# Kernel optimization log

Measured on AMD Instinct MI355X. Metric: run time of the kernel, lower is better.

## Reference

```python
import jax, jax.numpy as jnp
import numpy as np

ORDER = 25
L = ORDER + 1
K = 64
B = 262144
N_ITER = 8
WEIGHT_FLOOR = 1e-05
VAR_FLOOR = 1e-06
LOG_PI = L * float(np.log(2.0 * np.pi))  # (order+1)*log(2*pi)


def setup_inputs() -> dict:
    key = jax.random.key(0)
    k1, k2 = jax.random.split(key)
    x = jax.random.normal(k1, (B, L), dtype=jnp.float32)
    mu0 = jax.random.normal(k2, (K, L), dtype=jnp.float32)      # torch.randn(K, L)
    w0 = jnp.ones((K,), dtype=jnp.float32)                      # normalized to 1/K in reference
    sigma0 = jnp.ones((K, L), dtype=jnp.float32)                # diagonal of eye(L)
    return {"x": x, "w0": w0, "mu0": mu0, "sigma0": sigma0}


def _em_step(x, w, mu, sig):
    # ---- E-step (diag covariance path of the torch module) ----
    log_det = jnp.sum(jnp.log(sig), axis=-1)                    # [K]
    prec = 1.0 / sig                                            # [K,L]
    # mahala[b,k] = sum_l (x[b,l]-mu[k,l])^2 * prec[k,l]
    # expanded quadratic form to avoid materializing [B,K,L]
    mahala = ((x * x) @ prec.T
              - 2.0 * (x @ (mu * prec).T)
              + jnp.sum(mu * mu * prec, axis=-1))               # [B,K]
    numer = jnp.log(w) - 0.5 * (LOG_PI + log_det + mahala)      # [B,K]
    denom = jax.scipy.special.logsumexp(numer, axis=-1, keepdims=True)
    posterior = jnp.exp(numer - denom)                          # [B,K]
    ll = jnp.sum(denom)
    # ---- M-step (alpha == 0) ----
    z = jnp.sum(posterior, axis=0)                              # [K]
    w_new = z / B
    zinv = 1.0 / z
    # weight flooring + renormalization
    w_new = jnp.maximum(w_new, WEIGHT_FLOOR)
    sum_floor = WEIGHT_FLOOR * K
    a = (1.0 - sum_floor) / (jnp.sum(w_new) - sum_floor)
    b = WEIGHT_FLOOR * (1.0 - a)
    w_new = a * w_new + b
    px = posterior.T @ x                                        # [K,L]
    mu_new = px * zinv[:, None]
    pxx = posterior.T @ (x * x)                                 # [K,L]
    sig_new = pxx * zinv[:, None] - mu_new * mu_new
    sig_new = jnp.maximum(sig_new, VAR_FLOOR)                   # variance flooring
    return w_new, mu_new, sig_new, ll


def reference(x, w0, mu0, sigma0):
    w = w0 / jnp.sum(w0)                                        # == 1/K for ones init

    def body(carry, _):
        w, mu, sig, _ = carry
        w, mu, sig, ll = _em_step(x, w, mu, sig)
        return (w, mu, sig, ll), None

    init = (w, mu0, sigma0, jnp.zeros((), dtype=jnp.float32))
    (w, mu, sig, ll), _ = jax.lax.scan(body, init, None, length=N_ITER)
    sigma = jax.vmap(jnp.diag)(sig)                             # [K,L,L] diagonal covariances
    return w, mu, sigma, ll
```

## Files before the change

### kernel.cpp

```cpp
#include <hip/hip_runtime.h>
#include <math.h>

typedef _Float16 f16x2 __attribute__((ext_vector_type(2)));
typedef _Float16 f16x8 __attribute__((ext_vector_type(8)));
typedef float f32x16 __attribute__((ext_vector_type(16)));
typedef unsigned int uint4v __attribute__((ext_vector_type(4)));

namespace {
constexpr int LDIM = 26;
constexpr int KDIM = 64;
constexpr int NSAMP = 262144;
constexpr int NITER = 8;
constexpr float WFLOOR = 1e-5f;
constexpr float VFLOOR = 1e-6f;
constexpr float LOG2PI_TERM = 47.784803726642976f;
constexpr float L2E = 1.44269504088896340736f;
constexpr float LN2 = 0.69314718055994530942f;

constexpr int ACC_STRIDE = 53;
constexpr int ACC_N = KDIM * ACC_STRIDE + 1;
constexpr int NCOPIES = 8;
constexpr int WROW = 36;
constexpr int NBLK = 1024;
constexpr int PART_STRIDE = 3408;
constexpr int XROW = 20;
}

__device__ float g_partial[NBLK * PART_STRIDE];
__device__ float g_accum[NCOPIES * ACC_N];
__device__ float g_w[KDIM];
__device__ float g_mu[KDIM * LDIM];
__device__ float g_sig[KDIM * LDIM];
__device__ float g_ll[1];
__device__ __align__(16) unsigned g_coef[KDIM * WROW];
__device__ __align__(16) unsigned g_x16[NSAMP * XROW];

__device__ __forceinline__ unsigned pkrtz(float a, float b) {
  return __builtin_bit_cast(unsigned, __builtin_amdgcn_cvt_pkrtz(a, b));
}
__device__ __forceinline__ unsigned sqr16(unsigned u) {
  f16x2 a = __builtin_bit_cast(f16x2, u);
  a = a * a;
  return __builtin_bit_cast(unsigned, a);
}
__device__ __forceinline__ f16x8 ld8h(const unsigned* p) {
  uint4v v = *(const uint4v*)p;
  return __builtin_bit_cast(f16x8, v);
}
__device__ __forceinline__ f32x16 mfma16(f16x8 a, f16x8 b, f32x16 c) {
  return __builtin_amdgcn_mfma_f32_32x32x16_f16(a, b, c, 0, 0, 0);
}
__device__ __forceinline__ void gload16(const void* g, void* l) {
  __builtin_amdgcn_global_load_lds(
      (const __attribute__((address_space(1))) unsigned*)g,
      (__attribute__((address_space(3))) unsigned*)l, 16, 0, 0);
}

__device__ void pack_row(int k, float w, const float* mu, const float* sg, unsigned* wp) {
  float A[LDIM], Bv[LDIM];
  float logdet = 0.f, q = 0.f;
#pragma unroll
  for (int l = 0; l < LDIM; ++l) {
    float pr = 1.0f / sg[l];
    logdet += __logf(sg[l]);
    A[l] = -0.5f * pr;
    Bv[l] = mu[l] * pr;
    q = __builtin_fmaf(mu[l] * mu[l], pr, q);
  }
  float C = __logf(w) - 0.5f * (LOG2PI_TERM + logdet + q);
  float Chi = (float)__builtin_amdgcn_cvt_pkrtz(C, 0.0f)[0];
  float Clo = C - Chi;
  unsigned* row = wp + k * WROW;
#define CF(f) ((f) < 26 ? A[(f)] : (f) < 52 ? Bv[(f) - 26] : (f) == 52 ? C : (f) == 53 ? Clo : 0.0f)
#pragma unroll
  for (int D = 0; D < 32; ++D) row[D] = pkrtz(CF(2 * D), CF(2 * D + 1));
#undef CF
#pragma unroll
  for (int D = 32; D < 36; ++D) row[D] = 0u;
}

__global__ void prep_coef(const float* __restrict__ w0, const float* __restrict__ mu0,
                          const float* __restrict__ sig0) {
  const int k = threadIdx.x;
  float wv = w0[k];
  float s = wv;
#pragma unroll
  for (int d = 1; d < 64; d <<= 1) s += __shfl_xor(s, d, 64);
  float w = wv / s;
  float mu[LDIM], sg[LDIM];
#pragma unroll
  for (int l = 0; l < LDIM; ++l) {
    mu[l] = mu0[k * LDIM + l];
    sg[l] = sig0[k * LDIM + l];
  }
  pack_row(k, w, mu, sg, g_coef);
}

__global__ void pack16(const float* __restrict__ x) {
  const int total = NSAMP * XROW;
  for (int idx = blockIdx.x * 256 + threadIdx.x; idx < total; idx += gridDim.x * 256) {
    const int s = idx / XROW, j = idx % XROW;
    unsigned v = 0u;
    if (j < 13) {
      float2 p = *(const float2*)(x + (size_t)s * LDIM + 2 * j);
      v = pkrtz(p.x, p.y);
    }
    g_x16[idx] = v;
  }
}

__global__ __launch_bounds__(128, 2) void em_mfma() {
  __shared__ __align__(16) unsigned char pool[16384];
  __shared__ __align__(16) unsigned stage[2][2][32 * XROW];

  const int tid = threadIdx.x;
  const int lane = tid & 63;
  const int warp = tid >> 6;
  const int sl = lane & 31;
  const int h = lane >> 5;

  unsigned short* XTs = (unsigned short*)&pool[warp * 4096];
  unsigned short* SQs = (unsigned short*)&pool[warp * 4096 + 2048];
  unsigned short* PT0s = (unsigned short*)&pool[8192 + warp * 4096];
  unsigned short* PT1s = (unsigned short*)&pool[8192 + warp * 4096 + 2048];
  const unsigned* XTd = (const unsigned*)XTs;
  const unsigned* SQd = (const unsigned*)SQs;
  const unsigned* PT0d = (const unsigned*)PT0s;
  const unsigned* PT1d = (const unsigned*)PT1s;

  f32x16 aX0 = {0,0,0,0,0,0,0,0,0,0,0,0,0,0,0,0};
  f32x16 aX1 = {0,0,0,0,0,0,0,0,0,0,0,0,0,0,0,0};
  f32x16 aQ0 = {0,0,0,0,0,0,0,0,0,0,0,0,0,0,0,0};
  f32x16 aQ1 = {0,0,0,0,0,0,0,0,0,0,0,0,0,0,0,0};
  float llacc = 0.f;

  const int sbase = blockIdx.x * 256 + warp * 128;
  const int rowbase0 = sl * WROW;
  const int rowbase1 = (32 + sl) * WROW;

  f16x8 ca00 = ld8h(g_coef + rowbase0 + 0 + 4 * h);
  f16x8 ca01 = ld8h(g_coef + rowbase0 + 8 + 4 * h);
  f16x8 ca02 = ld8h(g_coef + rowbase0 + 16 + 4 * h);
  f16x8 ca03 = ld8h(g_coef + rowbase0 + 24 + 4 * h);
  f16x8 ca10 = ld8h(g_coef + rowbase1 + 0 + 4 * h);
  f16x8 ca11 = ld8h(g_coef + rowbase1 + 8 + 4 * h);
  f16x8 ca12 = ld8h(g_coef + rowbase1 + 16 + 4 * h);
  f16x8 ca13 = ld8h(g_coef + rowbase1 + 24 + 4 * h);

  auto stage_tile = [&](int tt) {
    const uint4v* tb = (const uint4v*)(g_x16 + (size_t)(sbase + 32 * tt) * XROW);
    char* db = (char*)&stage[warp][tt & 1][0];
    gload16(tb + lane, db + (size_t)lane * 16);
    gload16(tb + 64 + lane, db + 1024 + (size_t)lane * 16);
    if (lane < 32) gload16(tb + 128 + lane, db + 2048 + (size_t)lane * 16);
  };

  stage_tile(0);

#pragma unroll
  for (int t = 0; t < 4; ++t) {
    asm volatile("s_waitcnt vmcnt(0)" ::: "memory");

    if (t < 3) stage_tile(t + 1);

    unsigned xhu[13], squ[13];
    {
      const unsigned* srow = &stage[warp][t & 1][sl * XROW];
      uint4v r0 = *(const uint4v*)(srow);
      uint4v r1 = *(const uint4v*)(srow + 4);
      uint4v r2 = *(const uint4v*)(srow + 8);
      unsigned r12 = srow[12];
      xhu[0] = r0[0]; xhu[1] = r0[1]; xhu[2] = r0[2]; xhu[3] = r0[3];
      xhu[4] = r1[0]; xhu[5] = r1[1]; xhu[6] = r1[2]; xhu[7] = r1[3];
      xhu[8] = r2[0]; xhu[9] = r2[1]; xhu[10] = r2[2]; xhu[11] = r2[3];
      xhu[12] = r12;
#pragma unroll
      for (int j = 0; j < 13; ++j) squ[j] = sqr16(xhu[j]);
    }

    {
      unsigned short* Ts = h ? SQs : XTs;
#pragma unroll
      for (int c = 0; c < LDIM; ++c) {
        unsigned src = h ? squ[c >> 1] : xhu[c >> 1];
        unsigned v = (c & 1) ? (src >> 16) : (src & 0xffffu);
        Ts[(c * 32 + sl) ^ ((c & 7) << 3)] = (unsigned short)v;
      }
      Ts[(26 * 32 + sl) ^ ((26 & 7) << 3)] = h ? (unsigned short)0 : (unsigned short)0x3C00;
    }

    f32x16 e0 = {0,0,0,0,0,0,0,0,0,0,0,0,0,0,0,0};
    f32x16 e1 = {0,0,0,0,0,0,0,0,0,0,0,0,0,0,0,0};
    {
      uint4v b0 = {h ? squ[4] : squ[0], h ? squ[5] : squ[1],
                   h ? squ[6] : squ[2], h ? squ[7] : squ[3]};
      uint4v b1 = {h ? squ[12] : squ[8], h ? xhu[0] : squ[9],
                   h ? xhu[1] : squ[10], h ? xhu[2] : squ[11]};
      uint4v b2 = {h ? xhu[7] : xhu[3], h ? xhu[8] : xhu[4],
                   h ? xhu[9] : xhu[5], h ? xhu[10] : xhu[6]};
      uint4v b3 = {h ? 0u : xhu[11], h ? 0u : xhu[12],
                   h ? 0u : 0x3C003C00u, 0u};
      f16x8 fb0 = __builtin_bit_cast(f16x8, b0);
      f16x8 fb1 = __builtin_bit_cast(f16x8, b1);
      f16x8 fb2 = __builtin_bit_cast(f16x8, b2);
      f16x8 fb3 = __builtin_bit_cast(f16x8, b3);
      e0 = mfma16(ca00, fb0, e0);
      e1 = mfma16(ca10, fb0, e1);
      e0 = mfma16(ca01, fb1, e0);
      e1 = mfma16(ca11, fb1, e1);
      e0 = mfma16(ca02, fb2, e0);
      e1 = mfma16(ca12, fb2, e1);
      e0 = mfma16(ca03, fb3, e0);
      e1 = mfma16(ca13, fb3, e1);
    }

    float m8[8];
#pragma unroll
    for (int r = 0; r < 8; ++r)
      m8[r] = fmaxf(fmaxf(e0[r], e0[r + 8]), fmaxf(e1[r], e1[r + 8]));
#pragma unroll
    for (int d = 4; d > 0; d >>= 1)
#pragma unroll
      for (int r = 0; r < d; ++r) m8[r] = fmaxf(m8[r], m8[r + d]);
    const float M = fmaxf(m8[0], __shfl_xor(m8[0], 32));
    const float mL = M * L2E;
#pragma unroll
    for (int r = 0; r < 16; ++r) {
      e0[r] = __builtin_amdgcn_exp2f(__builtin_fmaf(e0[r], L2E, -mL));
      e1[r] = __builtin_amdgcn_exp2f(__builtin_fmaf(e1[r], L2E, -mL));
    }
    float s8[8];
#pragma unroll
    for (int r = 0; r < 8; ++r)
      s8[r] = (e0[r] + e0[r + 8]) + (e1[r] + e1[r + 8]);
#pragma unroll
    for (int d = 4; d > 0; d >>= 1)
#pragma unroll
      for (int r = 0; r < d; ++r) s8[r] += s8[r + d];
    const float SS = s8[0] + __shfl_xor(s8[0], 32);
    const float scale = __builtin_amdgcn_rcpf(SS);
    llacc += M + __builtin_amdgcn_logf(SS) * LN2;

#pragma unroll
    for (int r = 0; r < 16; ++r) {
      const int row = (r & 3) + 8 * (r >> 2) + 4 * h;
      const int idx = (row * 32 + sl) ^ ((row & 7) << 3);
      _Float16 p0 = (_Float16)(e0[r] * scale);
      _Float16 p1 = (_Float16)(e1[r] * scale);
      PT0s[idx] = __builtin_bit_cast(unsigned short, p0);
      PT1s[idx] = __builtin_bit_cast(unsigned short, p1);
    }

#pragma unroll
    for (int ks = 0; ks < 2; ++ks) {
      const int off = 8 * ks + 4 * h;
      const int swz = (sl & 7) << 2;
      f16x8 a0 = ld8h(&PT0d[(sl * 16 + off) ^ swz]);
      f16x8 a1 = ld8h(&PT1d[(sl * 16 + off) ^ swz]);
      f16x8 bx = ld8h(&XTd[(sl * 16 + off) ^ swz]);
      f16x8 bq = ld8h(&SQd[(sl * 16 + off) ^ swz]);
      aX0 = mfma16(a0, bx, aX0);
      aQ0 = mfma16(a0, bq, aQ0);
      aX1 = mfma16(a1, bx, aX1);
      aQ1 = mfma16(a1, bq, aQ1);
    }
  }

  __syncthreads();
  float* red = (float*)&pool[0];
  float llw = llacc * 0.5f;
#pragma unroll
  for (int d = 1; d < 64; d <<= 1) llw += __shfl_xor(llw, d, 64);
  if (warp == 0) {
#pragma unroll
    for (int r = 0; r < 16; ++r) {
      const int row = (r & 3) + 8 * (r >> 2) + 4 * h;
      if (sl < 26) {
        red[row * ACC_STRIDE + 1 + sl] = aX0[r];
        red[row * ACC_STRIDE + 27 + sl] = aQ0[r];
        red[(row + 32) * ACC_STRIDE + 1 + sl] = aX1[r];
        red[(row + 32) * ACC_STRIDE + 27 + sl] = aQ1[r];
      } else if (sl == 26) {
        red[row * ACC_STRIDE] = aX0[r];
        red[(row + 32) * ACC_STRIDE] = aX1[r];
      }
    }
    if (lane == 0) red[KDIM * ACC_STRIDE] = llw;
  }
  __syncthreads();
  if (warp == 1) {
    float* pb = g_partial + (size_t)blockIdx.x * PART_STRIDE;
#pragma unroll
    for (int r = 0; r < 16; ++r) {
      const int row = (r & 3) + 8 * (r >> 2) + 4 * h;
      if (sl < 26) {
        pb[row * ACC_STRIDE + 1 + sl] = red[row * ACC_STRIDE + 1 + sl] + aX0[r];
        pb[row * ACC_STRIDE + 27 + sl] = red[row * ACC_STRIDE + 27 + sl] + aQ0[r];
        pb[(row + 32) * ACC_STRIDE + 1 + sl] = red[(row + 32) * ACC_STRIDE + 1 + sl] + aX1[r];
        pb[(row + 32) * ACC_STRIDE + 27 + sl] = red[(row + 32) * ACC_STRIDE + 27 + sl] + aQ1[r];
      } else if (sl == 26) {
        pb[row * ACC_STRIDE] = red[row * ACC_STRIDE] + aX0[r];
        pb[(row + 32) * ACC_STRIDE] = red[(row + 32) * ACC_STRIDE] + aX1[r];
      }
    }
    if (lane == 0) pb[KDIM * ACC_STRIDE] = red[KDIM * ACC_STRIDE] + llw;
  }
}

__global__ void reduce_partials() {
  const int i = blockIdx.x * 256 + threadIdx.x;
  if (i >= ACC_N) return;
  const int cy = blockIdx.y;
  const float* p = g_partial + (size_t)cy * 128 * PART_STRIDE + i;
  float s = 0.f;
#pragma unroll 8
  for (int j = 0; j < 128; ++j) s += p[(size_t)j * PART_STRIDE];
  g_accum[cy * ACC_N + i] = s;
}

__global__ void finalize_k() {
  const int k = threadIdx.x;
  float vals[ACC_STRIDE];
#pragma unroll
  for (int j = 0; j < ACC_STRIDE; ++j) vals[j] = 0.f;
  float llsum = 0.f;
  for (int cp = 0; cp < NCOPIES; ++cp) {
    const float* a = g_accum + cp * ACC_N;
#pragma unroll
    for (int j = 0; j < ACC_STRIDE; ++j) vals[j] += a[k * ACC_STRIDE + j];
    llsum += a[KDIM * ACC_STRIDE];
  }
  float z = vals[0];
  float wn = z * (1.0f / NSAMP);
  float wf = fmaxf(wn, WFLOOR);
  float S = wf;
#pragma unroll
  for (int d = 1; d < 64; d <<= 1) S += __shfl_xor(S, d, 64);
  const float sf = WFLOOR * KDIM;
  float a = (1.0f - sf) / (S - sf);
  float b = WFLOOR * (1.0f - a);
  float w = a * wf + b;
  g_w[k] = w;
  float zinv = 1.0f / z;
  float muk[LDIM], sgk[LDIM];
#pragma unroll
  for (int l = 0; l < LDIM; ++l) {
    float m = vals[1 + l] * zinv;
    float s2 = fmaxf(__builtin_fmaf(-m, m, vals[27 + l] * zinv), VFLOOR);
    muk[l] = m;
    sgk[l] = s2;
    g_mu[k * LDIM + l] = m;
    g_sig[k * LDIM + l] = s2;
  }
  if (k == 0) g_ll[0] = llsum;
  pack_row(k, w, muk, sgk, g_coef);
}

__global__ void writeout(float* __restrict__ out) {
  const int i = blockIdx.x * 256 + threadIdx.x;
  if (i < 64) {
    out[i] = g_w[i];
  } else if (i < 64 + KDIM * LDIM) {
    out[i] = g_mu[i - 64];
  } else if (i < 64 + KDIM * LDIM + KDIM * LDIM * LDIM) {
    int t = i - (64 + KDIM * LDIM);
    int k = t / (LDIM * LDIM);
    int r = t % (LDIM * LDIM);
    int ii = r / LDIM;
    int jj = r % LDIM;
    out[i] = (ii == jj) ? g_sig[k * LDIM + ii] : 0.f;
  } else if (i == 64 + KDIM * LDIM + KDIM * LDIM * LDIM) {
    out[i] = g_ll[0];
  }
}

extern "C" void kernel_launch(void* const* d_in, const int* in_sizes, int n_in,
                              void* d_out, int out_size, void* d_ws, size_t ws_size,
                              hipStream_t stream) {
  (void)in_sizes; (void)n_in; (void)d_ws; (void)ws_size; (void)out_size;
  const float* x   = (const float*)d_in[0];
  const float* w0  = (const float*)d_in[1];
  const float* mu0 = (const float*)d_in[2];
  const float* sg0 = (const float*)d_in[3];
  float* out = (float*)d_out;

  prep_coef<<<1, 64, 0, stream>>>(w0, mu0, sg0);
  pack16<<<2048, 256, 0, stream>>>(x);
  for (int it = 0; it < NITER; ++it) {
    em_mfma<<<NBLK, 128, 0, stream>>>();
    reduce_partials<<<dim3(14, 8), 256, 0, stream>>>();
    finalize_k<<<1, 64, 0, stream>>>();
  }
  const int nout = 64 + KDIM * LDIM + KDIM * LDIM * LDIM + 1;
  writeout<<<(nout + 255) / 256, 256, 0, stream>>>(out);
}
```

Before: 318.9 us.

## Use four waves per block with direct register loads instead of LDS staging

The E/M-step kernel now runs 256 threads per block, with each wave handling 64 samples (two tiles) instead of 128 (four tiles). Samples go straight from global memory into registers, replacing the double-buffered global_load_lds staging. The block reduction becomes two parallel LDS pairwise reductions followed by a cooperative coalesced write of the partials. The aim is more waves in flight to hide latency and a cheaper, coalesced partial write-out, at the cost of more LDS per block and an extra barrier.

```diff
diff --git a/kernel.cpp b/kernel.cpp
--- a/kernel.cpp
+++ b/kernel.cpp
@@ -50,11 +50,6 @@
 __device__ __forceinline__ f32x16 mfma16(f16x8 a, f16x8 b, f32x16 c) {
   return __builtin_amdgcn_mfma_f32_32x32x16_f16(a, b, c, 0, 0, 0);
 }
-__device__ __forceinline__ void gload16(const void* g, void* l) {
-  __builtin_amdgcn_global_load_lds(
-      (const __attribute__((address_space(1))) unsigned*)g,
-      (__attribute__((address_space(3))) unsigned*)l, 16, 0, 0);
-}
 
 __device__ void pack_row(int k, float w, const float* mu, const float* sg, unsigned* wp) {
   float A[LDIM], Bv[LDIM];
@@ -109,9 +104,8 @@
   }
 }
 
-__global__ __launch_bounds__(128, 2) void em_mfma() {
-  __shared__ __align__(16) unsigned char pool[16384];
-  __shared__ __align__(16) unsigned stage[2][2][32 * XROW];
+__global__ __launch_bounds__(256, 3) void em_mfma() {
+  __shared__ __align__(16) unsigned char pool[32768];
 
   const int tid = threadIdx.x;
   const int lane = tid & 63;
@@ -119,10 +113,10 @@
   const int sl = lane & 31;
   const int h = lane >> 5;
 
-  unsigned short* XTs = (unsigned short*)&pool[warp * 4096];
-  unsigned short* SQs = (unsigned short*)&pool[warp * 4096 + 2048];
-  unsigned short* PT0s = (unsigned short*)&pool[8192 + warp * 4096];
-  unsigned short* PT1s = (unsigned short*)&pool[8192 + warp * 4096 + 2048];
+  unsigned short* XTs = (unsigned short*)&pool[warp * 8192];
+  unsigned short* SQs = (unsigned short*)&pool[warp * 8192 + 2048];
+  unsigned short* PT0s = (unsigned short*)&pool[warp * 8192 + 4096];
+  unsigned short* PT1s = (unsigned short*)&pool[warp * 8192 + 6144];
   const unsigned* XTd = (const unsigned*)XTs;
   const unsigned* SQd = (const unsigned*)SQs;
   const unsigned* PT0d = (const unsigned*)PT0s;
@@ -134,7 +128,7 @@
   f32x16 aQ1 = {0,0,0,0,0,0,0,0,0,0,0,0,0,0,0,0};
   float llacc = 0.f;
 
-  const int sbase = blockIdx.x * 256 + warp * 128;
+  const int sbase = blockIdx.x * 256 + warp * 64;
   const int rowbase0 = sl * WROW;
   const int rowbase1 = (32 + sl) * WROW;
 
@@ -147,36 +141,26 @@
   f16x8 ca12 = ld8h(g_coef + rowbase1 + 16 + 4 * h);
   f16x8 ca13 = ld8h(g_coef + rowbase1 + 24 + 4 * h);
 
-  auto stage_tile = [&](int tt) {
-    const uint4v* tb = (const uint4v*)(g_x16 + (size_t)(sbase + 32 * tt) * XROW);
-    char* db = (char*)&stage[warp][tt & 1][0];
-    gload16(tb + lane, db + (size_t)lane * 16);
-    gload16(tb + 64 + lane, db + 1024 + (size_t)lane * 16);
-    if (lane < 32) gload16(tb + 128 + lane, db + 2048 + (size_t)lane * 16);
-  };
-
-  stage_tile(0);
-
-#pragma unroll
-  for (int t = 0; t < 4; ++t) {
-    asm volatile("s_waitcnt vmcnt(0)" ::: "memory");
-
-    if (t < 3) stage_tile(t + 1);
-
+  uint4v ra[2][3];
+  unsigned rb[2];
+#pragma unroll
+  for (int t = 0; t < 2; ++t) {
+    const uint4v* rp = (const uint4v*)(g_x16 + (size_t)(sbase + 32 * t + sl) * XROW);
+    ra[t][0] = rp[0];
+    ra[t][1] = rp[1];
+    ra[t][2] = rp[2];
+    rb[t] = ((const unsigned*)rp)[12];
+  }
+
+#pragma unroll
+  for (int t = 0; t < 2; ++t) {
     unsigned xhu[13], squ[13];
-    {
-      const unsigned* srow = &stage[warp][t & 1][sl * XROW];
-      uint4v r0 = *(const uint4v*)(srow);
-      uint4v r1 = *(const uint4v*)(srow + 4);
-      uint4v r2 = *(const uint4v*)(srow + 8);
-      unsigned r12 = srow[12];
-      xhu[0] = r0[0]; xhu[1] = r0[1]; xhu[2] = r0[2]; xhu[3] = r0[3];
-      xhu[4] = r1[0]; xhu[5] = r1[1]; xhu[6] = r1[2]; xhu[7] = r1[3];
-      xhu[8] = r2[0]; xhu[9] = r2[1]; xhu[10] = r2[2]; xhu[11] = r2[3];
-      xhu[12] = r12;
-#pragma unroll
-      for (int j = 0; j < 13; ++j) squ[j] = sqr16(xhu[j]);
-    }
+    xhu[0] = ra[t][0][0]; xhu[1] = ra[t][0][1]; xhu[2] = ra[t][0][2]; xhu[3] = ra[t][0][3];
+    xhu[4] = ra[t][1][0]; xhu[5] = ra[t][1][1]; xhu[6] = ra[t][1][2]; xhu[7] = ra[t][1][3];
+    xhu[8] = ra[t][2][0]; xhu[9] = ra[t][2][1]; xhu[10] = ra[t][2][2]; xhu[11] = ra[t][2][3];
+    xhu[12] = rb[t];
+#pragma unroll
+    for (int j = 0; j < 13; ++j) squ[j] = sqr16(xhu[j]);
 
     {
       unsigned short* Ts = h ? SQs : XTs;
@@ -266,12 +250,15 @@
     }
   }
 
+  float* redA = (float*)&pool[0];
+  float* redB = (float*)&pool[16384];
+  float llw = llacc * 0.5f;
+#pragma unroll
+  for (int d = 1; d < 64; d <<= 1) llw += __shfl_xor(llw, d, 64);
+
   __syncthreads();
-  float* red = (float*)&pool[0];
-  float llw = llacc * 0.5f;
-#pragma unroll
-  for (int d = 1; d < 64; d <<= 1) llw += __shfl_xor(llw, d, 64);
-  if (warp == 0) {
+  if (warp == 0 || warp == 2) {
+    float* red = (warp == 0) ? redA : redB;
 #pragma unroll
     for (int r = 0; r < 16; ++r) {
       const int row = (r & 3) + 8 * (r >> 2) + 4 * h;
@@ -288,22 +275,27 @@
     if (lane == 0) red[KDIM * ACC_STRIDE] = llw;
   }
   __syncthreads();
-  if (warp == 1) {
-    float* pb = g_partial + (size_t)blockIdx.x * PART_STRIDE;
+  if (warp == 1 || warp == 3) {
+    float* red = (warp == 1) ? redA : redB;
 #pragma unroll
     for (int r = 0; r < 16; ++r) {
       const int row = (r & 3) + 8 * (r >> 2) + 4 * h;
       if (sl < 26) {
-        pb[row * ACC_STRIDE + 1 + sl] = red[row * ACC_STRIDE + 1 + sl] + aX0[r];
-        pb[row * ACC_STRIDE + 27 + sl] = red[row * ACC_STRIDE + 27 + sl] + aQ0[r];
-        pb[(row + 32) * ACC_STRIDE + 1 + sl] = red[(row + 32) * ACC_STRIDE + 1 + sl] + aX1[r];
-        pb[(row + 32) * ACC_STRIDE + 27 + sl] = red[(row + 32) * ACC_STRIDE + 27 + sl] + aQ1[r];
+        red[row * ACC_STRIDE + 1 + sl] += aX0[r];
+        red[row * ACC_STRIDE + 27 + sl] += aQ0[r];
+        red[(row + 32) * ACC_STRIDE + 1 + sl] += aX1[r];
+        red[(row + 32) * ACC_STRIDE + 27 + sl] += aQ1[r];
       } else if (sl == 26) {
-        pb[row * ACC_STRIDE] = red[row * ACC_STRIDE] + aX0[r];
-        pb[(row + 32) * ACC_STRIDE] = red[(row + 32) * ACC_STRIDE] + aX1[r];
+        red[row * ACC_STRIDE] += aX0[r];
+        red[(row + 32) * ACC_STRIDE] += aX1[r];
       }
     }
-    if (lane == 0) pb[KDIM * ACC_STRIDE] = red[KDIM * ACC_STRIDE] + llw;
+    if (lane == 0) red[KDIM * ACC_STRIDE] += llw;
+  }
+  __syncthreads();
+  {
+    float* pb = g_partial + (size_t)blockIdx.x * PART_STRIDE;
+    for (int i = tid; i < ACC_N; i += 256) pb[i] = redA[i] + redB[i];
   }
 }
 
@@ -387,7 +379,7 @@
   prep_coef<<<1, 64, 0, stream>>>(w0, mu0, sg0);
   pack16<<<2048, 256, 0, stream>>>(x);
   for (int it = 0; it < NITER; ++it) {
-    em_mfma<<<NBLK, 128, 0, stream>>>();
+    em_mfma<<<NBLK, 256, 0, stream>>>();
     reduce_partials<<<dim3(14, 8), 256, 0, stream>>>();
     finalize_k<<<1, 64, 0, stream>>>();
   }
```

Result: slower. 362.2 us (+13.6%).
